# Kernel optimization log

Measured on AMD Instinct MI355X. Metric: run time of the kernel, lower is better.

The kernel has to match this reference:

```python
import jax, jax.numpy as jnp
import numpy as np
from jax import lax

DEPTH, STACKS = 8, 2
C, SK, OUT = 64, 256, 256          # res_channels, skip_channels, out_channels
NB = DEPTH * STACKS                 # 16 blocks
DILS = [2 ** i for i in range(DEPTH)] * STACKS


def causal_conv(x, w, dil):
    # x: [B,C,T], w: [2C,C,2]; causal: left-pad by dil, kernel size 2 dilated
    return lax.conv_general_dilated(
        x, w, window_strides=(1,), padding=[(dil, 0)], rhs_dilation=(dil,),
        dimension_numbers=('NCH', 'OIH', 'NCH'))


def conv1x1(x, w):
    # x: [B,c_in,T], w: [c_out,c_in]
    return jnp.einsum('oc,bct->bot', w, x)


def setup_inputs() -> dict:
    key = jax.random.key(0)
    ks = jax.random.split(key, 8)
    B, T = 4, 8192
    x = jax.random.randint(ks[0], (B, T), 0, 256)
    h = jax.random.normal(ks[1], (B, NB * 2 * C, T), dtype=jnp.float32)
    embed = jax.random.normal(ks[2], (256, C), dtype=jnp.float32) * 0.1
    w_conv = jax.random.normal(ks[3], (NB, 2 * C, C, 2), dtype=jnp.float32) * 0.08
    w_res = jax.random.normal(ks[4], (NB, C, C), dtype=jnp.float32) * 0.08
    w_skip = jax.random.normal(ks[5], (NB, SK, C), dtype=jnp.float32) * 0.08
    w_out1 = jax.random.normal(ks[6], (OUT, SK), dtype=jnp.float32) * 0.05
    w_out2 = jax.random.normal(ks[7], (OUT, OUT), dtype=jnp.float32) * 0.05
    return {'x': x, 'h': h, 'embed': embed, 'w_conv': w_conv,
            'w_res': w_res, 'w_skip': w_skip, 'w_out1': w_out1, 'w_out2': w_out2}


def reference(x, h, embed, w_conv, w_res, w_skip, w_out1, w_out2):
    out = embed[x].transpose(0, 2, 1)          # [B,C,T]
    hs = jnp.split(h, NB, axis=1)              # NB chunks of [B,2C,T]
    skip = None
    for i in range(NB):
        g = causal_conv(out, w_conv[i], DILS[i]) + hs[i]   # [B,2C,T]
        z = jnp.tanh(g[:, :C]) * jax.nn.sigmoid(g[:, C:])  # gated activation
        s = conv1x1(z, w_skip[i])                          # [B,SK,T]
        skip = s if skip is None else skip + s
        if i < NB - 1:  # last block has return_residual=False (skip only)
            out = out + conv1x1(z, w_res[i])
    y = jax.nn.relu(skip)
    y = jax.nn.relu(conv1x1(y, w_out1))
    return conv1x1(y, w_out2)                  # [B,OUT,T]
```

## Files before the change

kernel.cpp:

```cpp
#include <hip/hip_runtime.h>

#define NB 16
#define TT 8192
#define Bb 4

typedef __attribute__((ext_vector_type(8))) short short8;
typedef __attribute__((ext_vector_type(16))) float f32x16;

__device__ __forceinline__ unsigned short bf16_rn(float f) {
  unsigned int u = __float_as_uint(f);
  u += 0x7FFF + ((u >> 16) & 1);
  return (unsigned short)(u >> 16);
}
__device__ __forceinline__ float bf16_to_f(unsigned short s) {
  return __uint_as_float(((unsigned int)s) << 16);
}
__device__ __forceinline__ unsigned int pack2(float a, float b) {
  return (unsigned int)bf16_rn(a) | ((unsigned int)bf16_rn(b) << 16);
}
__device__ __forceinline__ int kpos(int k) {
  int g = (k >> 2) & 1;
  int e = (k & 3) + 4 * (k >> 3);
  return g * 8 + e;
}
__device__ __forceinline__ int kinv(int p) {
  int g = p >> 3, e = p & 7;
  return (e & 3) + 4 * g + 8 * (e >> 2);
}

#define WINRD(base, r, off)                                                    \
  (*(const short8*)((char*)(base) +                                            \
      (((unsigned int)((r) * 128 + (off) * 2)) ^                               \
       ((unsigned int)(((r) & 7) << 4)))))

__global__ __launch_bounds__(256) void prep_weights(
    const float* __restrict__ wconv, const float* __restrict__ wres,
    const float* __restrict__ wsk, const float* __restrict__ w1,
    const float* __restrict__ w2, short* __restrict__ dwc,
    short* __restrict__ dwr, short* __restrict__ dws,
    short* __restrict__ dw1, short* __restrict__ dw2)
{
  int i = blockIdx.x * 256 + threadIdx.x;
  if (i < 262144) {
    int k = kinv(i & 15);
    int ic = (i & 48) | k;
    int oc = (i >> 6) & 127;
    int tap = (i >> 13) & 1;
    int blk = i >> 14;
    dwc[i] = (short)bf16_rn(wconv[(((blk * 128 + oc) * 64 + ic) << 1) | tap]);
    return;
  }
  int j = i - 262144;
  if (j < 65536) { dwr[j] = (short)bf16_rn(wres[(j & ~15) | kinv(j & 15)]); return; }
  j -= 65536;
  if (j < 262144) { dws[j] = (short)bf16_rn(wsk[(j & ~15) | kinv(j & 15)]); return; }
  j -= 262144;
  if (j < 65536) { dw1[j] = (short)bf16_rn(w1[(j & ~15) | kinv(j & 15)]); return; }
  j -= 65536;
  if (j < 65536) { dw2[j] = (short)bf16_rn(w2[(j & ~15) | kinv(j & 15)]); return; }
}

template <int DIL, int FIRST, int LAST>
__global__ __launch_bounds__(256) void block_kernel(
    const unsigned short* __restrict__ rin16, unsigned short* __restrict__ rout16,
    const int* __restrict__ x, const float* __restrict__ embed,
    const float* __restrict__ h, const short* __restrict__ wc,
    const short* __restrict__ wr, unsigned short* __restrict__ zg,
    int blk)
{
  __shared__ short win[2][(32 + DIL) * 64];
  __shared__ short zl[2][32 * 64];

  const int b = blockIdx.y;
  const int tile = threadIdx.x >> 7;
  const int htid = threadIdx.x & 127;
  const int t0 = (blockIdx.x * 2 + tile) * 32;
  const int lane = htid & 63, wv = htid >> 6;
  const int l31 = lane & 31, hi = lane >> 5;

  short* winT = win[tile];
  short* zlT = zl[tile];

  const int tcol = t0 + l31;
  f32x16 aA, aS;
  const float* hb = h + ((size_t)b * 2048 + (size_t)blk * 128) * TT;
#pragma unroll
  for (int r = 0; r < 16; ++r) {
    int row = (r & 3) + 4 * hi + 8 * (r >> 2) + 32 * wv;
    aA[r] = hb[(size_t)row * TT + tcol];
    aS[r] = hb[(size_t)(row + 64) * TT + tcol];
  }

  if (FIRST) {
    const int* xb = x + b * TT;
#pragma unroll
    for (int it = 0; it < 8; ++it) {
      int u = it * 128 + htid;
      int cpair = u & 31, t = u >> 5;
      int c0 = cpair * 2;
      int xi = xb[t0 + t];
      float v0 = embed[(size_t)xi * 64 + c0];
      float v1 = embed[(size_t)xi * 64 + c0 + 1];
      int p0 = (c0 & 48) | kpos(c0 & 15);
      int w = DIL + t;
      unsigned int byte = (unsigned int)(w * 128 + p0 * 2) ^
                          (unsigned int)((w & 7) << 4);
      *(unsigned int*)((char*)winT + byte) = pack2(v0, v1);
    }
    if (htid < 32) {
      int c0 = htid * 2;
      float v0 = 0.f, v1 = 0.f;
      if (t0 > 0) {
        int xi = xb[t0 - 1];
        v0 = embed[(size_t)xi * 64 + c0];
        v1 = embed[(size_t)xi * 64 + c0 + 1];
      }
      int p0 = (c0 & 48) | kpos(c0 & 15);
      unsigned int byte = (unsigned int)(p0 * 2);
      *(unsigned int*)((char*)winT + byte) = pack2(v0, v1);
    }
  } else {
    const unsigned short* rb16 = rin16 + (size_t)b * TT * 64;
#pragma unroll
    for (int it = 0; it < 2; ++it) {
      int u = it * 128 + htid;
      int q = u & 7, t = u >> 3;
      short8 v = *(const short8*)(rb16 + (size_t)(t0 + t) * 64 + q * 8);
      int w = DIL + t;
      unsigned int byte = (unsigned int)(w * 128 + q * 16) ^
                          (unsigned int)((w & 7) << 4);
      *(short8*)((char*)winT + byte) = v;
    }
    for (int u = htid; u < DIL * 8; u += 128) {
      int q = u & 7, w = u >> 3;
      int gt = t0 - DIL + w;
      short8 v = {};
      if (gt >= 0) v = *(const short8*)(rb16 + (size_t)gt * 64 + q * 8);
      unsigned int byte = (unsigned int)(w * 128 + q * 16) ^
                          (unsigned int)((w & 7) << 4);
      *(short8*)((char*)winT + byte) = v;
    }
  }
  __syncthreads();

  const short* wA0 = wc + (size_t)blk * 16384 + (32 * wv + l31) * 64;
  const short* wA1 = wA0 + 8192;
  const int r1 = DIL + l31;
  const int r0 = l31;
#pragma unroll
  for (int ks = 0; ks < 4; ++ks) {
    int off = ks * 16 + 8 * hi;
    short8 b1 = WINRD(winT, r1, off);
    short8 b0 = WINRD(winT, r0, off);
    short8 a0t = *(const short8*)(wA0 + off);
    short8 a1t = *(const short8*)(wA1 + off);
    short8 a0s = *(const short8*)(wA0 + 4096 + off);
    short8 a1s = *(const short8*)(wA1 + 4096 + off);
    aA = __builtin_amdgcn_mfma_f32_32x32x16_bf16(a0t, b0, aA, 0, 0, 0);
    aA = __builtin_amdgcn_mfma_f32_32x32x16_bf16(a1t, b1, aA, 0, 0, 0);
    aS = __builtin_amdgcn_mfma_f32_32x32x16_bf16(a0s, b0, aS, 0, 0, 0);
    aS = __builtin_amdgcn_mfma_f32_32x32x16_bf16(a1s, b1, aS, 0, 0, 0);
  }

#pragma unroll
  for (int r = 0; r < 16; r += 2) {
    int ic0 = (r & 3) + 4 * hi + 8 * (r >> 2) + 32 * wv;
    float z0 = (1.f - 2.f / (__expf(2.f * aA[r]) + 1.f)) *
               (1.f / (1.f + __expf(-aS[r])));
    float z1 = (1.f - 2.f / (__expf(2.f * aA[r + 1]) + 1.f)) *
               (1.f / (1.f + __expf(-aS[r + 1])));
    int p = (ic0 & ~15) | kpos(ic0 & 15);
    int tloc = l31;
    unsigned int byte = (unsigned int)(tloc * 128 + p * 2) ^
                        (unsigned int)((tloc & 7) << 4);
    *(unsigned int*)((char*)zlT + byte) = pack2(z0, z1);
  }
  __syncthreads();

  {
    unsigned short* zb = zg + ((size_t)(blk * Bb + b) * TT + t0) * 64;
#pragma unroll
    for (int it = 0; it < 8; ++it) {
      int u = it * 128 + htid;
      int p2 = u & 31, t = u >> 5;
      unsigned int byte = (unsigned int)(t * 128 + p2 * 4) ^
                          (unsigned int)((t & 7) << 4);
      unsigned int v = *(const unsigned int*)((char*)zlT + byte);
      *(unsigned int*)(zb + (size_t)t * 64 + p2 * 2) = v;
    }
  }

  if (!LAST) {
    const int trow = l31;
    f32x16 ar = {};
    const short* wrb = wr + (size_t)blk * 4096 + (wv * 32 + l31) * 64;
#pragma unroll
    for (int ks = 0; ks < 4; ++ks) {
      int off = ks * 16 + 8 * hi;
      short8 az = WINRD(zlT, trow, off);
      short8 bw = *(const short8*)(wrb + off);
      ar = __builtin_amdgcn_mfma_f32_32x32x16_bf16(az, bw, ar, 0, 0, 0);
    }
    unsigned short* obase = rout16 + (size_t)b * TT * 64;
    int oc = wv * 32 + l31;
    int ocp = (oc & 48) | kpos(oc & 15);
#pragma unroll
    for (int r = 0; r < 16; ++r) {
      int t = (r & 3) + 4 * hi + 8 * (r >> 2);
      int w = DIL + t;
      unsigned short ov = *(const unsigned short*)((char*)winT +
          (((unsigned int)(w * 128 + ocp * 2)) ^ ((unsigned int)((w & 7) << 4))));
      obase[(size_t)(t0 + t) * 64 + ocp] = bf16_rn(bf16_to_f(ov) + ar[r]);
    }
  }
}

__global__ __launch_bounds__(256) void head_kernel(
    const unsigned short* __restrict__ zg, const short* __restrict__ wsk,
    const short* __restrict__ w1, const short* __restrict__ w2,
    float* __restrict__ out)
{
  __shared__ short zbuf[2][32 * 64];
  __shared__ short yb[32 * 256];
  __shared__ short y2b[32 * 256];

  const int b = blockIdx.y;
  const int t0 = blockIdx.x * 32;
  const int tid = threadIdx.x;
  const int lane = tid & 63, wv = tid >> 6;
  const int l31 = lane & 31, hi = lane >> 5;

  {
#pragma unroll
    for (int it = 0; it < 4; ++it) {
      int u = it * 256 + tid;
      int p2 = u & 31, t = u >> 5;
      unsigned int v = *(const unsigned int*)(zg +
          ((size_t)(0 * Bb + b) * TT + t0 + t) * 64 + p2 * 2);
      unsigned int byte = (unsigned int)(t * 128 + p2 * 4) ^
                          (unsigned int)((t & 7) << 4);
      *(unsigned int*)((char*)zbuf[0] + byte) = v;
    }
  }

  f32x16 acc0 = {}, acc1 = {};
  const short* wsb0 = wsk + (wv * 32 + l31) * 64;
  const short* wsb1 = wsk + ((wv + 4) * 32 + l31) * 64;

  for (int blk = 0; blk < NB; ++blk) {
    __syncthreads();
    if (blk < NB - 1) {
#pragma unroll
      for (int it = 0; it < 4; ++it) {
        int u = it * 256 + tid;
        int p2 = u & 31, t = u >> 5;
        unsigned int v = *(const unsigned int*)(zg +
            ((size_t)((blk + 1) * Bb + b) * TT + t0 + t) * 64 + p2 * 2);
        unsigned int byte = (unsigned int)(t * 128 + p2 * 4) ^
                            (unsigned int)((t & 7) << 4);
        *(unsigned int*)((char*)zbuf[(blk + 1) & 1] + byte) = v;
      }
    }
    const short* zb = zbuf[blk & 1];
#pragma unroll
    for (int ks = 0; ks < 4; ++ks) {
      int off = ks * 16 + 8 * hi;
      short8 bw0 = *(const short8*)(wsb0 + (size_t)blk * 16384 + off);
      short8 bw1 = *(const short8*)(wsb1 + (size_t)blk * 16384 + off);
      short8 az = WINRD(zb, l31, off);
      acc0 = __builtin_amdgcn_mfma_f32_32x32x16_bf16(az, bw0, acc0, 0, 0, 0);
      acc1 = __builtin_amdgcn_mfma_f32_32x32x16_bf16(az, bw1, acc1, 0, 0, 0);
    }
  }

  {
    int sk0 = wv * 32 + l31;
    int sk1 = sk0 + 128;
    int p0 = (sk0 & 0xF0) | kpos(sk0 & 15);
    int p1 = (sk1 & 0xF0) | kpos(sk1 & 15);
#pragma unroll
    for (int r = 0; r < 16; ++r) {
      int dt = (r & 3) + 4 * hi + 8 * (r >> 2);
      unsigned int b0 = (unsigned int)(dt * 512 + p0 * 2) ^
                        (unsigned int)((dt & 7) << 4);
      unsigned int b1 = (unsigned int)(dt * 512 + p1 * 2) ^
                        (unsigned int)((dt & 7) << 4);
      *(short*)((char*)yb + b0) = (short)bf16_rn(fmaxf(acc0[r], 0.f));
      *(short*)((char*)yb + b1) = (short)bf16_rn(fmaxf(acc1[r], 0.f));
    }
  }
  __syncthreads();

#pragma unroll
  for (int ot = 0; ot < 2; ++ot) {
    const short* w1r = w1 + ((wv + 4 * ot) * 32 + l31) * 256;
    const int trow = l31;
    f32x16 acc = {};
#pragma unroll
    for (int ks = 0; ks < 16; ++ks) {
      int off = ks * 16 + 8 * hi;
      short8 by = *(const short8*)((char*)yb +
          ((unsigned int)(trow * 512 + off * 2) ^ (unsigned int)((trow & 7) << 4)));
      short8 aw = *(const short8*)(w1r + off);
      acc = __builtin_amdgcn_mfma_f32_32x32x16_bf16(aw, by, acc, 0, 0, 0);
    }
#pragma unroll
    for (int r = 0; r < 16; r += 2) {
      int o0 = (wv + 4 * ot) * 32 + (r & 3) + 4 * hi + 8 * (r >> 2);
      unsigned int v = (unsigned int)bf16_rn(fmaxf(acc[r], 0.f)) |
                       ((unsigned int)bf16_rn(fmaxf(acc[r + 1], 0.f)) << 16);
      int p = (o0 & 0xF0) | kpos(o0 & 15);
      unsigned int byte = (unsigned int)(trow * 512 + p * 2) ^
                          (unsigned int)((trow & 7) << 4);
      *(unsigned int*)((char*)y2b + byte) = v;
    }
  }
  __syncthreads();

  {
    float* ob = out + (size_t)b * 256 * TT;
#pragma unroll
    for (int ot = 0; ot < 2; ++ot) {
      const short* w2r = w2 + ((wv + 4 * ot) * 32 + l31) * 256;
      const int trow = l31;
      f32x16 acc = {};
#pragma unroll
      for (int ks = 0; ks < 16; ++ks) {
        int off = ks * 16 + 8 * hi;
        short8 by = *(const short8*)((char*)y2b +
            ((unsigned int)(trow * 512 + off * 2) ^ (unsigned int)((trow & 7) << 4)));
        short8 aw = *(const short8*)(w2r + off);
        acc = __builtin_amdgcn_mfma_f32_32x32x16_bf16(aw, by, acc, 0, 0, 0);
      }
#pragma unroll
      for (int r = 0; r < 16; ++r) {
        int oc = (wv + 4 * ot) * 32 + (r & 3) + 4 * hi + 8 * (r >> 2);
        ob[(size_t)oc * TT + t0 + trow] = acc[r];
      }
    }
  }
}

extern "C" void kernel_launch(void* const* d_in, const int* in_sizes, int n_in,
                              void* d_out, int out_size, void* d_ws, size_t ws_size,
                              hipStream_t stream)
{
  const int* x = (const int*)d_in[0];
  const float* h = (const float*)d_in[1];
  const float* embed = (const float*)d_in[2];
  const float* w_conv = (const float*)d_in[3];
  const float* w_res = (const float*)d_in[4];
  const float* w_skip = (const float*)d_in[5];
  const float* w_out1 = (const float*)d_in[6];
  const float* w_out2 = (const float*)d_in[7];
  float* out = (float*)d_out;

  char* ws = (char*)d_ws;
  unsigned short* r0 = (unsigned short*)ws;
  unsigned short* r1 = (unsigned short*)(ws + (size_t)(4 << 20));
  unsigned short* zg = (unsigned short*)(ws + (size_t)(8 << 20));
  short* dwc = (short*)(ws + (size_t)(72 << 20));
  short* dwr = dwc + 262144;
  short* dws = dwr + 65536;
  short* dw1 = dws + 262144;
  short* dw2 = dw1 + 65536;

  prep_weights<<<2816, 256, 0, stream>>>(w_conv, w_res, w_skip, w_out1, w_out2,
                                         dwc, dwr, dws, dw1, dw2);

  unsigned short* rf[2] = {r0, r1};
  const dim3 grid(TT / 64, Bb);

#define LAUNCH_BLK(DIL, FIRST, LAST, i)                                        \
  block_kernel<DIL, FIRST, LAST><<<grid, 256, 0, stream>>>(                    \
      rf[(i) & 1], rf[((i) + 1) & 1], x, embed, h, dwc, dwr, zg, (i))

  LAUNCH_BLK(1, 1, 0, 0);
  LAUNCH_BLK(2, 0, 0, 1);
  LAUNCH_BLK(4, 0, 0, 2);
  LAUNCH_BLK(8, 0, 0, 3);
  LAUNCH_BLK(16, 0, 0, 4);
  LAUNCH_BLK(32, 0, 0, 5);
  LAUNCH_BLK(64, 0, 0, 6);
  LAUNCH_BLK(128, 0, 0, 7);
  LAUNCH_BLK(1, 0, 0, 8);
  LAUNCH_BLK(2, 0, 0, 9);
  LAUNCH_BLK(4, 0, 0, 10);
  LAUNCH_BLK(8, 0, 0, 11);
  LAUNCH_BLK(16, 0, 0, 12);
  LAUNCH_BLK(32, 0, 0, 13);
  LAUNCH_BLK(64, 0, 0, 14);
  LAUNCH_BLK(128, 0, 1, 15);
#undef LAUNCH_BLK

  head_kernel<<<dim3(TT / 32, Bb), 256, 0, stream>>>(zg, dws, dw1, dw2, out);
}
```

Baseline: 323.7 us.

## Store activations pre-swizzled globally and stage tiles via direct global-to-LDS loads

```diff
diff --git a/kernel.cpp b/kernel.cpp
--- a/kernel.cpp
+++ b/kernel.cpp
@@ -28,10 +28,20 @@
   return (e & 3) + 4 * g + 8 * (e >> 2);
 }
 
+__device__ __forceinline__ void gload_lds16(const void* g, void* l) {
+  __builtin_amdgcn_global_load_lds(
+      (const __attribute__((address_space(1))) unsigned int*)g,
+      (__attribute__((address_space(3))) unsigned int*)l, 16, 0, 0);
+}
+
 #define WINRD(base, r, off)                                                    \
   (*(const short8*)((char*)(base) +                                            \
       (((unsigned int)((r) * 128 + (off) * 2)) ^                               \
        ((unsigned int)(((r) & 7) << 4)))))
+#define WINRDW(base, r, off, D)                                                \
+  (*(const short8*)((char*)(base) +                                            \
+      (((unsigned int)((r) * 128 + (off) * 2)) ^                               \
+       ((unsigned int)((((r) - (D)) & 7) << 4)))))
 
 __global__ __launch_bounds__(256) void prep_weights(
     const float* __restrict__ wconv, const float* __restrict__ wres,
@@ -68,8 +78,8 @@
     const short* __restrict__ wr, unsigned short* __restrict__ zg,
     int blk)
 {
-  __shared__ short win[2][(32 + DIL) * 64];
-  __shared__ short zl[2][32 * 64];
+  __shared__ __align__(16) short win[2][(32 + DIL) * 64];
+  __shared__ __align__(16) short zl[2][32 * 64];
 
   const int b = blockIdx.y;
   const int tile = threadIdx.x >> 7;
@@ -80,6 +90,33 @@
 
   short* winT = win[tile];
   short* zlT = zl[tile];
+
+  if (!FIRST) {
+    const char* rb16b = (const char*)(rin16 + (size_t)b * TT * 64);
+    if (t0 >= DIL) {
+      const char* gsrc = rb16b + (size_t)(t0 - DIL) * 128;
+      const int BYTES = (32 + DIL) * 128;
+      const int NCH = (BYTES + 1023) >> 10;
+      for (int c = wv; c < NCH; c += 2) {
+        int cb = c << 10;
+        if (cb + 1024 > BYTES) cb = BYTES - 1024;
+        gload_lds16(gsrc + cb + lane * 16, (char*)winT + cb);
+      }
+    } else {
+      for (int u = htid; u < (32 + DIL) * 8; u += 128) {
+        int q = u & 7, w = u >> 3;
+        int gt = t0 - DIL + w;
+        short8 v = {};
+        if (gt >= 0)
+          v = *(const short8*)(rb16b +
+              ((size_t)((unsigned int)(gt * 128 + q * 16) ^
+                        (unsigned int)((gt & 7) << 4))));
+        *(short8*)((char*)winT +
+            (((unsigned int)(w * 128 + q * 16)) ^
+             ((unsigned int)(((w - DIL) & 7) << 4)))) = v;
+      }
+    }
+  }
 
   const int tcol = t0 + l31;
   f32x16 aA, aS;
@@ -104,7 +141,7 @@
       int p0 = (c0 & 48) | kpos(c0 & 15);
       int w = DIL + t;
       unsigned int byte = (unsigned int)(w * 128 + p0 * 2) ^
-                          (unsigned int)((w & 7) << 4);
+                          (unsigned int)((t & 7) << 4);
       *(unsigned int*)((char*)winT + byte) = pack2(v0, v1);
     }
     if (htid < 32) {
@@ -116,29 +153,9 @@
         v1 = embed[(size_t)xi * 64 + c0 + 1];
       }
       int p0 = (c0 & 48) | kpos(c0 & 15);
-      unsigned int byte = (unsigned int)(p0 * 2);
+      unsigned int byte = (unsigned int)(p0 * 2) ^
+                          (unsigned int)((((0 - DIL) & 7)) << 4);
       *(unsigned int*)((char*)winT + byte) = pack2(v0, v1);
-    }
-  } else {
-    const unsigned short* rb16 = rin16 + (size_t)b * TT * 64;
-#pragma unroll
-    for (int it = 0; it < 2; ++it) {
-      int u = it * 128 + htid;
-      int q = u & 7, t = u >> 3;
-      short8 v = *(const short8*)(rb16 + (size_t)(t0 + t) * 64 + q * 8);
-      int w = DIL + t;
-      unsigned int byte = (unsigned int)(w * 128 + q * 16) ^
-                          (unsigned int)((w & 7) << 4);
-      *(short8*)((char*)winT + byte) = v;
-    }
-    for (int u = htid; u < DIL * 8; u += 128) {
-      int q = u & 7, w = u >> 3;
-      int gt = t0 - DIL + w;
-      short8 v = {};
-      if (gt >= 0) v = *(const short8*)(rb16 + (size_t)gt * 64 + q * 8);
-      unsigned int byte = (unsigned int)(w * 128 + q * 16) ^
-                          (unsigned int)((w & 7) << 4);
-      *(short8*)((char*)winT + byte) = v;
     }
   }
   __syncthreads();
@@ -150,8 +167,8 @@
 #pragma unroll
   for (int ks = 0; ks < 4; ++ks) {
     int off = ks * 16 + 8 * hi;
-    short8 b1 = WINRD(winT, r1, off);
-    short8 b0 = WINRD(winT, r0, off);
+    short8 b1 = WINRDW(winT, r1, off, DIL);
+    short8 b0 = WINRDW(winT, r0, off, DIL);
     short8 a0t = *(const short8*)(wA0 + off);
     short8 a1t = *(const short8*)(wA1 + off);
     short8 a0s = *(const short8*)(wA0 + 4096 + off);
@@ -178,15 +195,11 @@
   __syncthreads();
 
   {
-    unsigned short* zb = zg + ((size_t)(blk * Bb + b) * TT + t0) * 64;
+    char* zb = (char*)zg + (((size_t)(blk * Bb + b) * TT + t0) * 128);
 #pragma unroll
     for (int it = 0; it < 8; ++it) {
       int u = it * 128 + htid;
-      int p2 = u & 31, t = u >> 5;
-      unsigned int byte = (unsigned int)(t * 128 + p2 * 4) ^
-                          (unsigned int)((t & 7) << 4);
-      unsigned int v = *(const unsigned int*)((char*)zlT + byte);
-      *(unsigned int*)(zb + (size_t)t * 64 + p2 * 2) = v;
+      ((unsigned int*)zb)[u] = ((const unsigned int*)zlT)[u];
     }
   }
 
@@ -201,7 +214,7 @@
       short8 bw = *(const short8*)(wrb + off);
       ar = __builtin_amdgcn_mfma_f32_32x32x16_bf16(az, bw, ar, 0, 0, 0);
     }
-    unsigned short* obase = rout16 + (size_t)b * TT * 64;
+    char* ob = (char*)rout16 + (size_t)b * TT * 128;
     int oc = wv * 32 + l31;
     int ocp = (oc & 48) | kpos(oc & 15);
 #pragma unroll
@@ -209,8 +222,11 @@
       int t = (r & 3) + 4 * hi + 8 * (r >> 2);
       int w = DIL + t;
       unsigned short ov = *(const unsigned short*)((char*)winT +
-          (((unsigned int)(w * 128 + ocp * 2)) ^ ((unsigned int)((w & 7) << 4))));
-      obase[(size_t)(t0 + t) * 64 + ocp] = bf16_rn(bf16_to_f(ov) + ar[r]);
+          (((unsigned int)(w * 128 + ocp * 2)) ^
+           ((unsigned int)((t & 7) << 4))));
+      size_t byte = ((size_t)(t0 + t) * 128 + ocp * 2) ^
+                    (size_t)((t & 7) << 4);
+      *(unsigned short*)(ob + byte) = bf16_rn(bf16_to_f(ov) + ar[r]);
     }
   }
 }
@@ -220,9 +236,9 @@
     const short* __restrict__ w1, const short* __restrict__ w2,
     float* __restrict__ out)
 {
-  __shared__ short zbuf[2][32 * 64];
-  __shared__ short yb[32 * 256];
-  __shared__ short y2b[32 * 256];
+  __shared__ __align__(16) short zbuf[2][32 * 64];
+  __shared__ __align__(16) short yb[32 * 256];
+  __shared__ __align__(16) short y2b[32 * 256];
 
   const int b = blockIdx.y;
   const int t0 = blockIdx.x * 32;
@@ -231,16 +247,8 @@
   const int l31 = lane & 31, hi = lane >> 5;
 
   {
-#pragma unroll
-    for (int it = 0; it < 4; ++it) {
-      int u = it * 256 + tid;
-      int p2 = u & 31, t = u >> 5;
-      unsigned int v = *(const unsigned int*)(zg +
-          ((size_t)(0 * Bb + b) * TT + t0 + t) * 64 + p2 * 2);
-      unsigned int byte = (unsigned int)(t * 128 + p2 * 4) ^
-                          (unsigned int)((t & 7) << 4);
-      *(unsigned int*)((char*)zbuf[0] + byte) = v;
-    }
+    const char* zsrc = (const char*)zg + (((size_t)(0 * Bb + b) * TT + t0) * 128);
+    gload_lds16(zsrc + wv * 1024 + lane * 16, (char*)zbuf[0] + wv * 1024);
   }
 
   f32x16 acc0 = {}, acc1 = {};
@@ -250,16 +258,10 @@
   for (int blk = 0; blk < NB; ++blk) {
     __syncthreads();
     if (blk < NB - 1) {
-#pragma unroll
-      for (int it = 0; it < 4; ++it) {
-        int u = it * 256 + tid;
-        int p2 = u & 31, t = u >> 5;
-        unsigned int v = *(const unsigned int*)(zg +
-            ((size_t)((blk + 1) * Bb + b) * TT + t0 + t) * 64 + p2 * 2);
-        unsigned int byte = (unsigned int)(t * 128 + p2 * 4) ^
-                            (unsigned int)((t & 7) << 4);
-        *(unsigned int*)((char*)zbuf[(blk + 1) & 1] + byte) = v;
-      }
+      const char* zsrc = (const char*)zg +
+          (((size_t)((blk + 1) * Bb + b) * TT + t0) * 128);
+      gload_lds16(zsrc + wv * 1024 + lane * 16,
+                  (char*)zbuf[(blk + 1) & 1] + wv * 1024);
     }
     const short* zb = zbuf[blk & 1];
 #pragma unroll
```

Result: no change. 328.3 us (+1.4%).

## Prefetch next block's conditioning input as packed bf16 during current block

Applied to the files above, without the earlier changes.

```diff
diff --git a/kernel.cpp b/kernel.cpp
--- a/kernel.cpp
+++ b/kernel.cpp
@@ -32,6 +32,24 @@
   (*(const short8*)((char*)(base) +                                            \
       (((unsigned int)((r) * 128 + (off) * 2)) ^                               \
        ((unsigned int)(((r) & 7) << 4)))))
+
+__device__ __forceinline__ void conv_h_chunk(const float* __restrict__ hsrc,
+                                             unsigned short* __restrict__ dst,
+                                             int cls) {
+  const int rb = 4 * (cls & 1) + 32 * (cls >> 1);
+#pragma unroll
+  for (int jj = 0; jj < 8; ++jj) {
+    int row = ((2 * jj) & 3) + 8 * ((2 * jj) >> 2) + rb;
+    ((unsigned int*)dst)[jj] =
+        pack2(hsrc[(size_t)row * TT], hsrc[(size_t)(row + 1) * TT]);
+  }
+#pragma unroll
+  for (int jj = 0; jj < 8; ++jj) {
+    int row = 64 + ((2 * jj) & 3) + 8 * ((2 * jj) >> 2) + rb;
+    ((unsigned int*)dst)[8 + jj] =
+        pack2(hsrc[(size_t)row * TT], hsrc[(size_t)(row + 1) * TT]);
+  }
+}
 
 __global__ __launch_bounds__(256) void prep_weights(
     const float* __restrict__ wconv, const float* __restrict__ wres,
@@ -60,13 +78,27 @@
   if (j < 65536) { dw2[j] = (short)bf16_rn(w2[(j & ~15) | kinv(j & 15)]); return; }
 }
 
+__global__ __launch_bounds__(256) void prep_h0(
+    const float* __restrict__ h, unsigned short* __restrict__ h16p)
+{
+  int idx = blockIdx.x * 256 + threadIdx.x;
+  int tc = idx & 8191;
+  int cls = (idx >> 13) & 3;
+  int b = idx >> 15;
+  const float* hsrc = h + (size_t)b * 2048 * TT + tc;
+  unsigned short* dst =
+      h16p + (((size_t)(b * NB + 0) * 4 + cls) * TT + tc) * 32;
+  conv_h_chunk(hsrc, dst, cls);
+}
+
 template <int DIL, int FIRST, int LAST>
 __global__ __launch_bounds__(256) void block_kernel(
     const unsigned short* __restrict__ rin16, unsigned short* __restrict__ rout16,
     const int* __restrict__ x, const float* __restrict__ embed,
-    const float* __restrict__ h, const short* __restrict__ wc,
-    const short* __restrict__ wr, unsigned short* __restrict__ zg,
-    int blk)
+    const float* __restrict__ h, const unsigned short* __restrict__ h16p,
+    unsigned short* __restrict__ h16w,
+    const short* __restrict__ wc, const short* __restrict__ wr,
+    unsigned short* __restrict__ zg, int blk)
 {
   __shared__ short win[2][(32 + DIL) * 64];
   __shared__ short zl[2][32 * 64];
@@ -81,14 +113,20 @@
   short* winT = win[tile];
   short* zlT = zl[tile];
 
-  const int tcol = t0 + l31;
+  const int cls = wv * 2 + hi;
+  const unsigned short* hp =
+      h16p + ((((size_t)(b * NB + blk) * 4 + cls) * TT + (size_t)(t0 + l31)) * 32);
+  short8 hq0 = *(const short8*)(hp);
+  short8 hq1 = *(const short8*)(hp + 8);
+  short8 hq2 = *(const short8*)(hp + 16);
+  short8 hq3 = *(const short8*)(hp + 24);
   f32x16 aA, aS;
-  const float* hb = h + ((size_t)b * 2048 + (size_t)blk * 128) * TT;
-#pragma unroll
-  for (int r = 0; r < 16; ++r) {
-    int row = (r & 3) + 4 * hi + 8 * (r >> 2) + 32 * wv;
-    aA[r] = hb[(size_t)row * TT + tcol];
-    aS[r] = hb[(size_t)(row + 64) * TT + tcol];
+#pragma unroll
+  for (int r = 0; r < 8; ++r) {
+    aA[r] = bf16_to_f((unsigned short)hq0[r]);
+    aA[r + 8] = bf16_to_f((unsigned short)hq1[r]);
+    aS[r] = bf16_to_f((unsigned short)hq2[r]);
+    aS[r + 8] = bf16_to_f((unsigned short)hq3[r]);
   }
 
   if (FIRST) {
@@ -212,6 +250,17 @@
           (((unsigned int)(w * 128 + ocp * 2)) ^ ((unsigned int)((w & 7) << 4))));
       obase[(size_t)(t0 + t) * 64 + ocp] = bf16_rn(bf16_to_f(ov) + ar[r]);
     }
+  }
+
+  if (!LAST) {
+    const int tb = blockIdx.x * 64;
+    const int tcl = threadIdx.x & 63;
+    const int tcls = threadIdx.x >> 6;
+    const int tc = tb + tcl;
+    const float* hsrc = h + ((size_t)b * 2048 + (size_t)(blk + 1) * 128) * TT + tc;
+    unsigned short* dst =
+        h16w + (((size_t)(b * NB + blk + 1) * 4 + tcls) * TT + tc) * 32;
+    conv_h_chunk(hsrc, dst, tcls);
   }
 }
 
@@ -359,7 +408,8 @@
   unsigned short* r0 = (unsigned short*)ws;
   unsigned short* r1 = (unsigned short*)(ws + (size_t)(4 << 20));
   unsigned short* zg = (unsigned short*)(ws + (size_t)(8 << 20));
-  short* dwc = (short*)(ws + (size_t)(72 << 20));
+  unsigned short* h16p = (unsigned short*)(ws + (size_t)(72 << 20));
+  short* dwc = (short*)(ws + (size_t)(200 << 20));
   short* dwr = dwc + 262144;
   short* dws = dwr + 65536;
   short* dw1 = dws + 262144;
@@ -367,13 +417,14 @@
 
   prep_weights<<<2816, 256, 0, stream>>>(w_conv, w_res, w_skip, w_out1, w_out2,
                                          dwc, dwr, dws, dw1, dw2);
+  prep_h0<<<512, 256, 0, stream>>>(h, h16p);
 
   unsigned short* rf[2] = {r0, r1};
   const dim3 grid(TT / 64, Bb);
 
 #define LAUNCH_BLK(DIL, FIRST, LAST, i)                                        \
   block_kernel<DIL, FIRST, LAST><<<grid, 256, 0, stream>>>(                    \
-      rf[(i) & 1], rf[((i) + 1) & 1], x, embed, h, dwc, dwr, zg, (i))
+      rf[(i) & 1], rf[((i) + 1) & 1], x, embed, h, h16p, h16p, dwc, dwr, zg, (i))
 
   LAUNCH_BLK(1, 1, 0, 0);
   LAUNCH_BLK(2, 0, 0, 1);
```

Result: slower. 388.6 us (+20.1%).
